# Optimization experiments

Measured on AMD Instinct MI355X. Metric: run time of the kernel, lower is better.

## Reference

```python
import jax, jax.numpy as jnp
import numpy as np


def setup_inputs() -> dict:
    key = jax.random.key(0)
    ks = jax.random.split(key, 12)
    M, B, N, FD, BD, BVD, H = 4096, 8, 512, 128, 128, 6, 64
    return {
        "f_pre_in": jax.random.normal(ks[0], (M, FD), jnp.float32),
        "f_pre_batch": jnp.sort(jax.random.randint(ks[1], (M,), 0, B)),
        "b_pre_in": jax.random.normal(ks[2], (B, BD, N), jnp.float32),
        "bv_in": jax.random.normal(ks[3], (B, BVD, N), jnp.float32),
        "Wf": jax.random.normal(ks[4], (H, FD), jnp.float32) * 0.05,
        "bf": jax.random.normal(ks[5], (H,), jnp.float32) * 0.05,
        "Wb": jax.random.normal(ks[6], (H, BD), jnp.float32) * 0.05,
        "bb": jax.random.normal(ks[7], (H,), jnp.float32) * 0.05,
        "Wbv": jax.random.normal(ks[8], (H, BVD), jnp.float32) * 0.05,
        "bbv": jax.random.normal(ks[9], (H,), jnp.float32) * 0.05,
        "Wo": jax.random.normal(ks[10], (H, 2 * H), jnp.float32) * 0.05,
        "bo": jax.random.normal(ks[11], (H,), jnp.float32) * 0.05,
    }


def reference(f_pre_in, f_pre_batch, b_pre_in, bv_in, Wf, bf, Wb, bb, Wbv, bbv, Wo, bo):
    # 1x1 Conv1d == channel matmul.
    H = Wf.shape[0]
    h2 = H // 2
    scale = jnp.sqrt(jnp.asarray(H, jnp.float32))  # sqrt(hidden_size)
    f = Wf @ f_pre_in.T + bf[:, None]                                  # (H, M)
    b_feat = jnp.einsum('hd,bdn->bhn', Wb, b_pre_in) + bb[None, :, None]   # (B, H, N)
    bv_feat = jnp.einsum('hc,bcn->bhn', Wbv, bv_in) + bbv[None, :, None]   # (B, H, N)
    # Per-node gather of that node's graph boundary features (f_pre_batch is sorted,
    # so per-node order == torch's per-batch concat order).
    be = b_feat[f_pre_batch, :h2]    # (M, h2, N)
    bg = b_feat[f_pre_batch, h2:]    # (M, h2, N)
    bvg = bv_feat[f_pre_batch]       # (M, H, N)
    # Cross-attention: softmax over the N boundary positions (torch dim=0 of (N, n_b)).
    w_euc = jax.nn.softmax(jnp.einsum('mhn,hm->mn', be, f[:h2]) / scale, axis=-1)  # (M, N)
    w_geo = jax.nn.softmax(jnp.einsum('mhn,hm->mn', bg, f[h2:]) / scale, axis=-1)  # (M, N)
    out_euc = jnp.einsum('mhn,mn->mh', bvg, w_euc)   # (M, H)
    out_geo = jnp.einsum('mhn,mn->mh', bvg, w_geo)   # (M, H)
    cat = jnp.concatenate([out_euc, out_geo], axis=1)  # (M, 2H)
    return cat @ Wo.T + bo                              # (M, H)
```

## Files before the change

### kernel.cpp

```cpp
#include <hip/hip_runtime.h>

#define M_TOT 4096
#define B_TOT 8
#define N_TOT 512
#define FD    128
#define BD    128
#define BVD   6
#define H     64
#define H2    32
#define MAX_TILES 264

__device__ __forceinline__ int lb_dev(const int* __restrict__ arr, int n, int v) {
    int lo = 0, hi = n;
    while (lo < hi) { int mid = (lo + hi) >> 1; if (arr[mid] < v) lo = mid + 1; else hi = mid; }
    return lo;
}

__global__ __launch_bounds__(256) void k_pre(const float* __restrict__ f_pre_in,
                                             const int*   __restrict__ batch,
                                             const float* __restrict__ b_pre_in,
                                             const float* __restrict__ bv_in,
                                             const float* __restrict__ Wf,
                                             const float* __restrict__ bf,
                                             const float* __restrict__ Wb,
                                             const float* __restrict__ bb,
                                             const float* __restrict__ Wbv,
                                             const float* __restrict__ bbv,
                                             float* __restrict__ f_mh,
                                             float* __restrict__ b_feat,
                                             float* __restrict__ bv_T,
                                             int4*  __restrict__ table) {
    __shared__ float fpre[16 * 132];
    __shared__ float WfT[128 * 68];
    __shared__ float ws2[2 * 132];
    const int t = threadIdx.x;
    const int blk = blockIdx.x;

    if (blk < 256) {
        const int m0 = blk * 16;
        for (int i = t; i < 16 * FD; i += 256)
            fpre[(i >> 7) * 132 + (i & 127)] = f_pre_in[(size_t)m0 * FD + i];
        for (int i = t; i < H * FD; i += 256)
            WfT[(i & 127) * 68 + (i >> 7)] = Wf[i];
        __syncthreads();
        const int mi = t >> 4;
        const int h4 = (t & 15) * 4;
        float a0 = bf[h4], a1 = bf[h4 + 1], a2 = bf[h4 + 2], a3 = bf[h4 + 3];
#pragma unroll 4
        for (int d4 = 0; d4 < 32; ++d4) {
            const float4 fp = *(const float4*)&fpre[mi * 132 + d4 * 4];
            const float* fpp = &fp.x;
#pragma unroll
            for (int i = 0; i < 4; ++i) {
                const float4 wv = *(const float4*)&WfT[(d4 * 4 + i) * 68 + h4];
                const float f = fpp[i];
                a0 += f * wv.x; a1 += f * wv.y; a2 += f * wv.z; a3 += f * wv.w;
            }
        }
        *(float4*)&f_mh[(size_t)(m0 + mi) * H + h4] = make_float4(a0, a1, a2, a3);
    } else if (blk < 512) {
        const int idx = blk - 256;
        const int b  = idx >> 5;
        const int h0 = (idx & 31) * 2;
        ws2[(t >> 7) * 132 + (t & 127)] = Wb[(h0 + (t >> 7)) * BD + (t & 127)];
        __syncthreads();
        const int hi = t >> 7;
        const int n4 = (t & 127) * 4;
        const float bias = bb[h0 + hi];
        float a0 = bias, a1 = bias, a2 = bias, a3 = bias;
        const float* src = b_pre_in + (size_t)b * BD * N_TOT + n4;
        const float* wp = &ws2[hi * 132];
#pragma unroll 8
        for (int d = 0; d < BD; ++d) {
            const float wv = wp[d];
            const float4 v = *(const float4*)(src + (size_t)d * N_TOT);
            a0 += wv * v.x; a1 += wv * v.y; a2 += wv * v.z; a3 += wv * v.w;
        }
        *(float4*)&b_feat[((size_t)b * H + h0 + hi) * N_TOT + n4] = make_float4(a0, a1, a2, a3);
    } else if (blk < 768) {
        const int idx = blk - 512;
        const int b  = idx >> 5;
        const int n0 = (idx & 31) * 16;
        const int h  = t & 63;
        const int nq = t >> 6;
        float wreg[BVD];
#pragma unroll
        for (int c = 0; c < BVD; ++c) wreg[c] = Wbv[h * BVD + c];
        const float bias = bbv[h];
        const float* src = bv_in + (size_t)b * BVD * N_TOT;
#pragma unroll
        for (int j = 0; j < 4; ++j) {
            const int n = n0 + nq * 4 + j;
            float acc = bias;
#pragma unroll
            for (int c = 0; c < BVD; ++c) acc += wreg[c] * src[c * N_TOT + n];
            bv_T[((size_t)b * N_TOT + n) * H + h] = acc;
        }
    } else {
        int starts[9];
#pragma unroll
        for (int b = 0; b <= 8; ++b) starts[b] = lb_dev(batch, M_TOT, b);
        int pre[9]; pre[0] = 0;
#pragma unroll
        for (int b = 0; b < 8; ++b) pre[b + 1] = pre[b] + (starts[b + 1] - starts[b] + 15) / 16;
        const int total = pre[8];
        for (int idx = t; idx < MAX_TILES; idx += 256) {
            int4 e = make_int4(0, 0, 0, 0);
            if (idx < total) {
                int b = 0;
                while (pre[b + 1] <= idx) ++b;
                const int r0 = starts[b] + (idx - pre[b]) * 16;
                e.x = b; e.y = r0; e.z = min(16, starts[b + 1] - r0);
            }
            table[idx] = e;
        }
    }
}

__device__ __forceinline__ float wave_sum64(float x) {
#pragma unroll
    for (int m = 1; m < 64; m <<= 1) x += __shfl_xor(x, m);
    return x;
}

__global__ __launch_bounds__(512, 4) void k_main(const float* __restrict__ f_mh,
                                                 const float* __restrict__ b_feat,
                                                 const float* __restrict__ bv_T,
                                                 const int4*  __restrict__ table,
                                                 float* __restrict__ pOut,
                                                 float* __restrict__ pSum) {
    __shared__ float fT[64 * 20];
    __shared__ float bFbv[64 * 133];
    __shared__ float wE[16 * 132];
    __shared__ float wG[16 * 132];
    __shared__ float rowsum[16][2];

    const int t = threadIdx.x;
    const int q    = blockIdx.x & 3;
    const int tile = blockIdx.x >> 2;
    const int4 te = table[tile];
    const int b = te.x, m0 = te.y, nr = te.z;
    if (nr == 0) return;
    const int nb = q * 128;

    for (int i = t; i < 16 * H; i += 512) {
        const int r = i >> 6, h = i & 63;
        fT[h * 20 + r] = f_mh[(size_t)(m0 + min(r, nr - 1)) * H + h];
    }
    {
        const float* src = b_feat + (size_t)b * H * N_TOT + nb;
        for (int i = t; i < 2048; i += 512) {
            const int h = i >> 5, n4 = (i & 31) * 4;
            *(float4*)&bFbv[h * 132 + n4] = *(const float4*)&src[(size_t)h * N_TOT + n4];
        }
    }
    if (t < 32) rowsum[t >> 1][t & 1] = 0.f;
    __syncthreads();

    const int lane = t & 63;
    {
        const int n_l = t & 127;
        const int rgs = t >> 7;
        float se[4] = {0.f, 0.f, 0.f, 0.f}, sg[4] = {0.f, 0.f, 0.f, 0.f};
#pragma unroll 8
        for (int h = 0; h < H2; ++h) {
            const float bE = bFbv[h * 132 + n_l];
            const float bG = bFbv[(h + 32) * 132 + n_l];
            const float4 fe = *(const float4*)&fT[h * 20 + rgs * 4];
            const float4 fg = *(const float4*)&fT[(h + 32) * 20 + rgs * 4];
            se[0] += fe.x * bE; se[1] += fe.y * bE; se[2] += fe.z * bE; se[3] += fe.w * bE;
            sg[0] += fg.x * bG; sg[1] += fg.y * bG; sg[2] += fg.z * bG; sg[3] += fg.w * bG;
        }
        float we[4], wg[4];
#pragma unroll
        for (int j = 0; j < 4; ++j) {
            we[j] = __expf(se[j] * 0.125f);
            wg[j] = __expf(sg[j] * 0.125f);
        }
#pragma unroll
        for (int j = 0; j < 4; ++j) {
            const float sE = wave_sum64(we[j]);
            const float sG = wave_sum64(wg[j]);
            if (lane == 0) {
                atomicAdd(&rowsum[rgs * 4 + j][0], sE);
                atomicAdd(&rowsum[rgs * 4 + j][1], sG);
            }
            wE[(rgs * 4 + j) * 132 + n_l] = we[j];
            wG[(rgs * 4 + j) * 132 + n_l] = wg[j];
        }
    }
    __syncthreads();

    {
        const float* src = bv_T + ((size_t)b * N_TOT + nb) * H;
        for (int i = t; i < 2048; i += 512) {
            const int n_li = i >> 4, h4 = (i & 15) * 4;
            const float4 v = *(const float4*)&src[(size_t)n_li * H + h4];
            bFbv[(h4 + 0) * 133 + n_li] = v.x;
            bFbv[(h4 + 1) * 133 + n_li] = v.y;
            bFbv[(h4 + 2) * 133 + n_li] = v.z;
            bFbv[(h4 + 3) * 133 + n_li] = v.w;
        }
    }
    __syncthreads();

    if (t < 32) {
        const int r = t >> 1, eg = t & 1;
        if (r < nr) pSum[((size_t)q * M_TOT + m0 + r) * 2 + eg] = rowsum[r][eg];
    }

    {
        const int ns = t & 3, hg = (t >> 2) & 15, rgp = t >> 6;
        float aE[2][4] = {{0.f,0.f,0.f,0.f},{0.f,0.f,0.f,0.f}};
        float aG[2][4] = {{0.f,0.f,0.f,0.f},{0.f,0.f,0.f,0.f}};
#pragma unroll 4
        for (int i = 0; i < 32; ++i) {
            const int n = ns + 4 * i;
            const float we0 = wE[(rgp * 2 + 0) * 132 + n];
            const float we1 = wE[(rgp * 2 + 1) * 132 + n];
            const float wg0 = wG[(rgp * 2 + 0) * 132 + n];
            const float wg1 = wG[(rgp * 2 + 1) * 132 + n];
            float bv4[4];
#pragma unroll
            for (int c = 0; c < 4; ++c) bv4[c] = bFbv[(hg * 4 + c) * 133 + n];
#pragma unroll
            for (int c = 0; c < 4; ++c) {
                aE[0][c] += we0 * bv4[c];
                aE[1][c] += we1 * bv4[c];
                aG[0][c] += wg0 * bv4[c];
                aG[1][c] += wg1 * bv4[c];
            }
        }
#pragma unroll
        for (int j = 0; j < 2; ++j)
#pragma unroll
            for (int c = 0; c < 4; ++c) {
                aE[j][c] += __shfl_xor(aE[j][c], 1); aE[j][c] += __shfl_xor(aE[j][c], 2);
                aG[j][c] += __shfl_xor(aG[j][c], 1); aG[j][c] += __shfl_xor(aG[j][c], 2);
            }
        if (ns == 0) {
#pragma unroll
            for (int j = 0; j < 2; ++j) {
                const int r = rgp * 2 + j;
                if (r < nr) {
                    float* dst = pOut + ((size_t)q * M_TOT + m0 + r) * 128;
                    *(float4*)&dst[hg * 4]      = make_float4(aE[j][0], aE[j][1], aE[j][2], aE[j][3]);
                    *(float4*)&dst[64 + hg * 4] = make_float4(aG[j][0], aG[j][1], aG[j][2], aG[j][3]);
                }
            }
        }
    }
}

__global__ __launch_bounds__(256) void k_merge(const float* __restrict__ pOut,
                                               const float* __restrict__ pSum,
                                               const float* __restrict__ Wo,
                                               const float* __restrict__ bo,
                                               float* __restrict__ out) {
    __shared__ float WoT[128 * 68];
    __shared__ float cat[16 * 132];
    __shared__ float rinv[16][2];
    const int t = threadIdx.x;
    const int m0 = blockIdx.x * 16;

    for (int i = t; i < H * 2 * H; i += 256)
        WoT[(i & 127) * 68 + (i >> 7)] = Wo[i];
    if (t < 32) {
        const int r = t >> 1, eg = t & 1;
        float s = 0.f;
#pragma unroll
        for (int qq = 0; qq < 4; ++qq) s += pSum[((size_t)qq * M_TOT + m0 + r) * 2 + eg];
        rinv[r][eg] = 1.0f / s;
    }
    __syncthreads();

    for (int i = t; i < 512; i += 256) {
        const int r = i >> 5, k4 = (i & 31) * 4;
        float4 s = make_float4(0.f, 0.f, 0.f, 0.f);
#pragma unroll
        for (int qq = 0; qq < 4; ++qq) {
            const float4 v = *(const float4*)&pOut[(((size_t)qq * M_TOT + m0 + r) * 128) + k4];
            s.x += v.x; s.y += v.y; s.z += v.z; s.w += v.w;
        }
        const float inv = rinv[r][k4 >= 64];
        *(float4*)&cat[r * 132 + k4] = make_float4(s.x * inv, s.y * inv, s.z * inv, s.w * inv);
    }
    __syncthreads();

    const int mi = t >> 4;
    const int j4 = (t & 15) * 4;
    float a0 = bo[j4], a1 = bo[j4 + 1], a2 = bo[j4 + 2], a3 = bo[j4 + 3];
#pragma unroll 4
    for (int k4s = 0; k4s < 32; ++k4s) {
        const float4 c4 = *(const float4*)&cat[mi * 132 + 4 * k4s];
        const float* cp = &c4.x;
#pragma unroll
        for (int i = 0; i < 4; ++i) {
            const float4 wv = *(const float4*)&WoT[(4 * k4s + i) * 68 + j4];
            const float c = cp[i];
            a0 += c * wv.x; a1 += c * wv.y; a2 += c * wv.z; a3 += c * wv.w;
        }
    }
    *(float4*)&out[(size_t)(m0 + mi) * H + j4] = make_float4(a0, a1, a2, a3);
}

extern "C" void kernel_launch(void* const* d_in, const int* in_sizes, int n_in,
                              void* d_out, int out_size, void* d_ws, size_t ws_size,
                              hipStream_t stream) {
    const float* f_pre_in = (const float*)d_in[0];
    const int*   f_batch  = (const int*)  d_in[1];
    const float* b_pre_in = (const float*)d_in[2];
    const float* bv_in    = (const float*)d_in[3];
    const float* Wf       = (const float*)d_in[4];
    const float* bf       = (const float*)d_in[5];
    const float* Wb       = (const float*)d_in[6];
    const float* bb       = (const float*)d_in[7];
    const float* Wbv      = (const float*)d_in[8];
    const float* bbv      = (const float*)d_in[9];
    const float* Wo       = (const float*)d_in[10];
    const float* bo       = (const float*)d_in[11];
    float* out = (float*)d_out;

    float* f_mh   = (float*)d_ws;
    float* b_feat = f_mh + (size_t)M_TOT * H;
    float* bv_T   = b_feat + (size_t)B_TOT * H * N_TOT;
    float* pOut   = bv_T + (size_t)B_TOT * N_TOT * H;
    float* pSum   = pOut + (size_t)4 * M_TOT * 128;
    int4*  table  = (int4*)(pSum + (size_t)4 * M_TOT * 2);

    k_pre  <<<769, 256, 0, stream>>>(f_pre_in, f_batch, b_pre_in, bv_in,
                                     Wf, bf, Wb, bb, Wbv, bbv,
                                     f_mh, b_feat, bv_T, table);
    k_main <<<4 * MAX_TILES, 512, 0, stream>>>(f_mh, b_feat, bv_T, table, pOut, pSum);
    k_merge<<<256, 256, 0, stream>>>(pOut, pSum, Wo, bo, out);
}
```

Baseline: 135.5 us.

## Register-tile score and weighted-sum phases with float4 LDS reads in k_main

Restructures both compute phases of k_main into 4x4 register tiles. The score phase splits the H reduction across 4 lanes and reduces with shuffles. The weights are stored transposed (n-major) so the accumulation phase can read float4 weight and value vectors, and bv is now staged row-major in a padded buffer instead of being scattered into a transposed layout. The goal is fewer LDS loads per FMA and no scalar transposing stores, at the cost of extra shuffle reductions and higher register pressure.

```diff
diff --git a/kernel.cpp b/kernel.cpp
--- a/kernel.cpp
+++ b/kernel.cpp
@@ -117,22 +117,16 @@
     }
 }
 
-__device__ __forceinline__ float wave_sum64(float x) {
-#pragma unroll
-    for (int m = 1; m < 64; m <<= 1) x += __shfl_xor(x, m);
-    return x;
-}
-
 __global__ __launch_bounds__(512, 4) void k_main(const float* __restrict__ f_mh,
                                                  const float* __restrict__ b_feat,
                                                  const float* __restrict__ bv_T,
                                                  const int4*  __restrict__ table,
                                                  float* __restrict__ pOut,
                                                  float* __restrict__ pSum) {
+    __shared__ float sbuf[128 * 72];
+    __shared__ float wTe[128 * 20 + 4];
+    __shared__ float wTg[128 * 20 + 4];
     __shared__ float fT[64 * 20];
-    __shared__ float bFbv[64 * 133];
-    __shared__ float wE[16 * 132];
-    __shared__ float wG[16 * 132];
     __shared__ float rowsum[16][2];
 
     const int t = threadIdx.x;
@@ -143,50 +137,90 @@
     if (nr == 0) return;
     const int nb = q * 128;
 
+    if (t < 32) rowsum[t >> 1][t & 1] = 0.f;
     for (int i = t; i < 16 * H; i += 512) {
-        const int r = i >> 6, h = i & 63;
+        const int h = i & 63, r = i >> 6;
         fT[h * 20 + r] = f_mh[(size_t)(m0 + min(r, nr - 1)) * H + h];
     }
     {
         const float* src = b_feat + (size_t)b * H * N_TOT + nb;
         for (int i = t; i < 2048; i += 512) {
             const int h = i >> 5, n4 = (i & 31) * 4;
-            *(float4*)&bFbv[h * 132 + n4] = *(const float4*)&src[(size_t)h * N_TOT + n4];
-        }
-    }
-    if (t < 32) rowsum[t >> 1][t & 1] = 0.f;
-    __syncthreads();
-
-    const int lane = t & 63;
-    {
-        const int n_l = t & 127;
-        const int rgs = t >> 7;
-        float se[4] = {0.f, 0.f, 0.f, 0.f}, sg[4] = {0.f, 0.f, 0.f, 0.f};
-#pragma unroll 8
-        for (int h = 0; h < H2; ++h) {
-            const float bE = bFbv[h * 132 + n_l];
-            const float bG = bFbv[(h + 32) * 132 + n_l];
-            const float4 fe = *(const float4*)&fT[h * 20 + rgs * 4];
-            const float4 fg = *(const float4*)&fT[(h + 32) * 20 + rgs * 4];
-            se[0] += fe.x * bE; se[1] += fe.y * bE; se[2] += fe.z * bE; se[3] += fe.w * bE;
-            sg[0] += fg.x * bG; sg[1] += fg.y * bG; sg[2] += fg.z * bG; sg[3] += fg.w * bG;
-        }
-        float we[4], wg[4];
+            *(float4*)&sbuf[h * 132 + n4] = *(const float4*)&src[(size_t)h * N_TOT + n4];
+        }
+    }
+    __syncthreads();
+
+    const int hq = t & 3;
+    const int nq = (t >> 2) & 31;
+    const int rg = t >> 7;
+    const int n4 = nq * 4;
+    const int r4 = rg * 4;
+
+    float se[4][4], sg[4][4];
+#pragma unroll
+    for (int j = 0; j < 4; ++j)
+#pragma unroll
+        for (int r = 0; r < 4; ++r) { se[j][r] = 0.f; sg[j][r] = 0.f; }
+#pragma unroll
+    for (int hh = 0; hh < 8; ++hh) {
+        const int h = hh * 4 + hq;
+        const float4 fr = *(const float4*)&fT[h * 20 + r4];
+        const float4 bn = *(const float4*)&sbuf[h * 132 + n4];
+        const float* frp = &fr.x; const float* bnp = &bn.x;
+#pragma unroll
+        for (int j = 0; j < 4; ++j)
+#pragma unroll
+            for (int r = 0; r < 4; ++r) se[j][r] += bnp[j] * frp[r];
+    }
+#pragma unroll
+    for (int hh = 0; hh < 8; ++hh) {
+        const int h = 32 + hh * 4 + hq;
+        const float4 fr = *(const float4*)&fT[h * 20 + r4];
+        const float4 bn = *(const float4*)&sbuf[h * 132 + n4];
+        const float* frp = &fr.x; const float* bnp = &bn.x;
+#pragma unroll
+        for (int j = 0; j < 4; ++j)
+#pragma unroll
+            for (int r = 0; r < 4; ++r) sg[j][r] += bnp[j] * frp[r];
+    }
+#pragma unroll
+    for (int j = 0; j < 4; ++j)
+#pragma unroll
+        for (int r = 0; r < 4; ++r) {
+            float v = se[j][r]; v += __shfl_xor(v, 1); v += __shfl_xor(v, 2); se[j][r] = v;
+            float u = sg[j][r]; u += __shfl_xor(u, 1); u += __shfl_xor(u, 2); sg[j][r] = u;
+        }
+    float we_[4][4], wg_[4][4];
+    float pe[4] = {0.f, 0.f, 0.f, 0.f}, pg[4] = {0.f, 0.f, 0.f, 0.f};
+#pragma unroll
+    for (int j = 0; j < 4; ++j)
+#pragma unroll
+        for (int r = 0; r < 4; ++r) {
+            we_[j][r] = __expf(se[j][r] * 0.125f); pe[r] += we_[j][r];
+            wg_[j][r] = __expf(sg[j][r] * 0.125f); pg[r] += wg_[j][r];
+        }
+#pragma unroll
+    for (int r = 0; r < 4; ++r) {
+        float v = pe[r];
+        v += __shfl_xor(v, 4); v += __shfl_xor(v, 8); v += __shfl_xor(v, 16); v += __shfl_xor(v, 32);
+        pe[r] = v;
+        float u = pg[r];
+        u += __shfl_xor(u, 4); u += __shfl_xor(u, 8); u += __shfl_xor(u, 16); u += __shfl_xor(u, 32);
+        pg[r] = u;
+    }
+    if ((t & 63) == 0) {
+#pragma unroll
+        for (int r = 0; r < 4; ++r) {
+            atomicAdd(&rowsum[r4 + r][0], pe[r]);
+            atomicAdd(&rowsum[r4 + r][1], pg[r]);
+        }
+    }
+    if (hq == 0) {
 #pragma unroll
         for (int j = 0; j < 4; ++j) {
-            we[j] = __expf(se[j] * 0.125f);
-            wg[j] = __expf(sg[j] * 0.125f);
-        }
-#pragma unroll
-        for (int j = 0; j < 4; ++j) {
-            const float sE = wave_sum64(we[j]);
-            const float sG = wave_sum64(wg[j]);
-            if (lane == 0) {
-                atomicAdd(&rowsum[rgs * 4 + j][0], sE);
-                atomicAdd(&rowsum[rgs * 4 + j][1], sG);
-            }
-            wE[(rgs * 4 + j) * 132 + n_l] = we[j];
-            wG[(rgs * 4 + j) * 132 + n_l] = wg[j];
+            *(float4*)&wTe[(n4 + j) * 20 + r4] = make_float4(we_[j][0], we_[j][1], we_[j][2], we_[j][3]);
+            *(float4*)&wTg[(n4 + j) * 20 + r4] = make_float4(wg_[j][0], wg_[j][1], wg_[j][2], wg_[j][3]);
         }
     }
     __syncthreads();
@@ -194,12 +228,8 @@
     {
         const float* src = bv_T + ((size_t)b * N_TOT + nb) * H;
         for (int i = t; i < 2048; i += 512) {
-            const int n_li = i >> 4, h4 = (i & 15) * 4;
-            const float4 v = *(const float4*)&src[(size_t)n_li * H + h4];
-            bFbv[(h4 + 0) * 133 + n_li] = v.x;
-            bFbv[(h4 + 1) * 133 + n_li] = v.y;
-            bFbv[(h4 + 2) * 133 + n_li] = v.z;
-            bFbv[(h4 + 3) * 133 + n_li] = v.w;
+            const int n = i >> 4, h4s = (i & 15) * 4;
+            *(float4*)&sbuf[n * 72 + h4s] = *(const float4*)&src[(size_t)n * H + h4s];
         }
     }
     __syncthreads();
@@ -209,44 +239,42 @@
         if (r < nr) pSum[((size_t)q * M_TOT + m0 + r) * 2 + eg] = rowsum[r][eg];
     }
 
-    {
-        const int ns = t & 3, hg = (t >> 2) & 15, rgp = t >> 6;
-        float aE[2][4] = {{0.f,0.f,0.f,0.f},{0.f,0.f,0.f,0.f}};
-        float aG[2][4] = {{0.f,0.f,0.f,0.f},{0.f,0.f,0.f,0.f}};
-#pragma unroll 4
-        for (int i = 0; i < 32; ++i) {
-            const int n = ns + 4 * i;
-            const float we0 = wE[(rgp * 2 + 0) * 132 + n];
-            const float we1 = wE[(rgp * 2 + 1) * 132 + n];
-            const float wg0 = wG[(rgp * 2 + 0) * 132 + n];
-            const float wg1 = wG[(rgp * 2 + 1) * 132 + n];
-            float bv4[4];
-#pragma unroll
-            for (int c = 0; c < 4; ++c) bv4[c] = bFbv[(hg * 4 + c) * 133 + n];
+    const int ns = t & 7;
+    const int h4 = ((t >> 3) & 15) * 4;
+    float aE[4][4], aG[4][4];
+#pragma unroll
+    for (int r = 0; r < 4; ++r)
+#pragma unroll
+        for (int c = 0; c < 4; ++c) { aE[r][c] = 0.f; aG[r][c] = 0.f; }
+#pragma unroll
+    for (int i = 0; i < 16; ++i) {
+        const int n = ns + 8 * i;
+        const float4 w4e = *(const float4*)&wTe[n * 20 + r4];
+        const float4 w4g = *(const float4*)&wTg[n * 20 + r4];
+        const float4 v4  = *(const float4*)&sbuf[n * 72 + h4];
+        const float* wep = &w4e.x; const float* wgp = &w4g.x; const float* vp = &v4.x;
+#pragma unroll
+        for (int r = 0; r < 4; ++r)
 #pragma unroll
             for (int c = 0; c < 4; ++c) {
-                aE[0][c] += we0 * bv4[c];
-                aE[1][c] += we1 * bv4[c];
-                aG[0][c] += wg0 * bv4[c];
-                aG[1][c] += wg1 * bv4[c];
+                aE[r][c] += wep[r] * vp[c];
+                aG[r][c] += wgp[r] * vp[c];
             }
-        }
-#pragma unroll
-        for (int j = 0; j < 2; ++j)
-#pragma unroll
-            for (int c = 0; c < 4; ++c) {
-                aE[j][c] += __shfl_xor(aE[j][c], 1); aE[j][c] += __shfl_xor(aE[j][c], 2);
-                aG[j][c] += __shfl_xor(aG[j][c], 1); aG[j][c] += __shfl_xor(aG[j][c], 2);
-            }
-        if (ns == 0) {
-#pragma unroll
-            for (int j = 0; j < 2; ++j) {
-                const int r = rgp * 2 + j;
-                if (r < nr) {
-                    float* dst = pOut + ((size_t)q * M_TOT + m0 + r) * 128;
-                    *(float4*)&dst[hg * 4]      = make_float4(aE[j][0], aE[j][1], aE[j][2], aE[j][3]);
-                    *(float4*)&dst[64 + hg * 4] = make_float4(aG[j][0], aG[j][1], aG[j][2], aG[j][3]);
-                }
+    }
+#pragma unroll
+    for (int r = 0; r < 4; ++r)
+#pragma unroll
+        for (int c = 0; c < 4; ++c) {
+            float v = aE[r][c]; v += __shfl_xor(v, 1); v += __shfl_xor(v, 2); v += __shfl_xor(v, 4); aE[r][c] = v;
+            float u = aG[r][c]; u += __shfl_xor(u, 1); u += __shfl_xor(u, 2); u += __shfl_xor(u, 4); aG[r][c] = u;
+        }
+    if (ns == 0) {
+#pragma unroll
+        for (int j = 0; j < 4; ++j) {
+            if (r4 + j < nr) {
+                float* dst = pOut + ((size_t)q * M_TOT + m0 + r4 + j) * 128;
+                *(float4*)&dst[h4]      = make_float4(aE[j][0], aE[j][1], aE[j][2], aE[j][3]);
+                *(float4*)&dst[64 + h4] = make_float4(aG[j][0], aG[j][1], aG[j][2], aG[j][3]);
             }
         }
     }
```

After: 141.8 us. 4.6% more time.
